# Kernel optimization log

Hardware: AMD Instinct MI355X
Metric: run time of the kernel (lower is better)

The kernel has to match this reference:

```python
import jax, jax.numpy as jnp
import numpy as np

# ---- static problem configuration (matches init_kwargs) ----
N_PAIRS = 256
NODES_PER_GRAPH = 64
EDGES_PER_GRAPH = 200
MAX_EDGES = 256            # max_edge_set_size
N_GRAPHS = 2 * N_PAIRS     # query/corpus interleaved
N_NODES = N_GRAPHS * NODES_PER_GRAPH
N_EDGES = N_GRAPHS * EDGES_PER_GRAPH
NODE_DIM = 16
EDGE_DIM = 16
H = 128                    # node_state_dim
E_ENC = 64                 # encoded edge feature dim
MSG = 256                  # edge_hidden_sizes[-1] = 2*H (GMN GRU convention)
SK = 32                    # sinkhorn_feature_dim
PROP_STEPS = 5
SK_ITERS = 20
TEMP = 0.1


def setup_inputs() -> dict:
    key = jax.random.key(0)
    ks = jax.random.split(key, 16)
    node_features = jax.random.normal(ks[0], (N_NODES, NODE_DIM), jnp.float32)
    edge_features = jax.random.normal(ks[1], (N_EDGES, EDGE_DIM), jnp.float32)
    # edges are grouped per graph (graph g owns edges [g*E, (g+1)*E)) and
    # endpoints stay inside graph g's node range, as get_graph_features assumes
    offs = np.repeat(np.arange(N_GRAPHS) * NODES_PER_GRAPH, EDGES_PER_GRAPH)
    rng = np.random.default_rng(0)
    from_idx = jnp.asarray(offs + rng.integers(0, NODES_PER_GRAPH, N_EDGES), jnp.int32)
    to_idx = jnp.asarray(offs + rng.integers(0, NODES_PER_GRAPH, N_EDGES), jnp.int32)

    def lin(k, i, o):
        return jax.random.normal(k, (i, o), jnp.float32) / np.sqrt(i).astype(np.float32)

    p = dict(
        enc_node_w=lin(ks[2], NODE_DIM, H), enc_node_b=jnp.zeros((H,), jnp.float32),
        enc_edge_w=lin(ks[3], EDGE_DIM, E_ENC), enc_edge_b=jnp.zeros((E_ENC,), jnp.float32),
        msg_w1=lin(ks[4], 2 * H + E_ENC, MSG), msg_b1=jnp.zeros((MSG,), jnp.float32),
        msg_w2=lin(ks[5], MSG, MSG), msg_b2=jnp.zeros((MSG,), jnp.float32),
        rmsg_w1=lin(ks[6], 2 * H + E_ENC, MSG), rmsg_b1=jnp.zeros((MSG,), jnp.float32),
        rmsg_w2=lin(ks[7], MSG, MSG), rmsg_b2=jnp.zeros((MSG,), jnp.float32),
        gru_w_ih=lin(ks[8], MSG, 3 * H), gru_b_ih=jnp.zeros((3 * H,), jnp.float32),
        gru_w_hh=lin(ks[9], H, 3 * H), gru_b_hh=jnp.zeros((3 * H,), jnp.float32),
        sk_w1=lin(ks[10], MSG, SK), sk_b1=jnp.zeros((SK,), jnp.float32),
        sk_w2=lin(ks[11], SK, SK), sk_b2=jnp.zeros((SK,), jnp.float32),
    )
    return {"node_features": node_features, "edge_features": edge_features,
            "from_idx": from_idx, "to_idx": to_idx, **p}


def _mlp2(x, w1, b1, w2, b2):
    # Linear -> ReLU -> Linear (GMN MLP: no activation after last layer)
    return jax.nn.relu(x @ w1 + b1) @ w2 + b2


def reference(node_features, edge_features, from_idx, to_idx,
              enc_node_w, enc_node_b, enc_edge_w, enc_edge_b,
              msg_w1, msg_b1, msg_w2, msg_b2,
              rmsg_w1, rmsg_b1, rmsg_w2, rmsg_b2,
              gru_w_ih, gru_b_ih, gru_w_hh, gru_b_hh,
              sk_w1, sk_b1, sk_w2, sk_b2):
    # ---- GraphEncoder (single-layer MLPs) ----
    h = node_features @ enc_node_w + enc_node_b          # [N_NODES, H]
    e = edge_features @ enc_edge_w + enc_edge_b          # [N_EDGES, E_ENC]

    def edge_msgs(h):
        s, d = h[from_idx], h[to_idx]                    # gathers [N_EDGES, H]
        fwd = _mlp2(jnp.concatenate([s, d, e], axis=1), msg_w1, msg_b1, msg_w2, msg_b2)
        rev = _mlp2(jnp.concatenate([d, s, e], axis=1), rmsg_w1, rmsg_b1, rmsg_w2, rmsg_b2)
        return fwd, rev                                  # [N_EDGES, MSG] each

    # ---- propagation loop: gather -> edge MLP -> scatter -> GRU update ----
    for _ in range(PROP_STEPS):
        fwd, rev = edge_msgs(h)
        agg = (jax.ops.segment_sum(fwd, to_idx, num_segments=N_NODES)
               + jax.ops.segment_sum(rev, from_idx, num_segments=N_NODES))  # [N_NODES, MSG]
        gi = agg @ gru_w_ih + gru_b_ih                   # [N_NODES, 3H]
        gh = h @ gru_w_hh + gru_b_hh
        r = jax.nn.sigmoid(gi[:, :H] + gh[:, :H])
        z = jax.nn.sigmoid(gi[:, H:2 * H] + gh[:, H:2 * H])
        n = jnp.tanh(gi[:, 2 * H:] + r * gh[:, 2 * H:])
        h = (1.0 - z) * n + z * h                        # torch GRU update

    # ---- propagation_messages: per-edge fwd + rev message ----
    fwd, rev = edge_msgs(h)
    e_final = fwd + rev                                  # [N_EDGES, MSG]

    # ---- split_and_stack: per-graph edge sets padded to MAX_EDGES ----
    stacked = jnp.pad(e_final.reshape(N_GRAPHS, EDGES_PER_GRAPH, MSG),
                      ((0, 0), (0, MAX_EDGES - EDGES_PER_GRAPH), (0, 0)))
    q, c = stacked[0::2], stacked[1::2]                  # [B, MAX_EDGES, MSG]

    # ---- sinkhorn feature MLP + size mask ----
    tq = _mlp2(q, sk_w1, sk_b1, sk_w2, sk_b2)            # [B, MAX_EDGES, SK]
    tc = _mlp2(c, sk_w1, sk_b1, sk_w2, sk_b2)
    mask = (jnp.arange(MAX_EDGES) < EDGES_PER_GRAPH).astype(jnp.float32)[None, :, None]
    mq, mc = mask * tq, mask * tc

    # ---- log-domain Sinkhorn ----
    la = jnp.einsum('bif,bjf->bij', mq, mc) / TEMP       # [B, MAX_EDGES, MAX_EDGES]
    for _ in range(SK_ITERS):
        la = la - jax.nn.logsumexp(la, axis=2, keepdims=True)
        la = la - jax.nn.logsumexp(la, axis=1, keepdims=True)
    plan = jnp.exp(la)

    # ---- feature_alignment_score: -sum relu(q - P @ c) ----
    return -jnp.sum(jax.nn.relu(q - jnp.einsum('bij,bjf->bif', plan, c)), axis=(1, 2))
```

## Files before the change

kernel.cpp:

```cpp
#include <hip/hip_runtime.h>
#include <math.h>

typedef __attribute__((ext_vector_type(4))) float f32x4;
typedef __attribute__((ext_vector_type(8))) short s16x8;
typedef __attribute__((ext_vector_type(4))) short s16x4;

#define NN 32768
#define NE 102400
#define HD 128
#define EED 64
#define MSGD 256
#define NG 512
#define EPG 200
#define NP 256
#define SKD 32

__device__ inline short f2bf(float x){
  union{float f; unsigned u;} z; z.f=x;
  unsigned r = (z.u + 0x7fffu + ((z.u>>16)&1u)) >> 16;
  return (short)r;
}
__device__ inline float bf2f(unsigned short u){
  union{unsigned u; float f;} z; z.u = ((unsigned)u)<<16; return z.f;
}
__device__ inline float frcp(float x){
  float r; asm("v_rcp_f32 %0, %1" : "=v"(r) : "v"(x)); return r;
}

__global__ void __launch_bounds__(256) k_enc_node(const float* __restrict__ nf,
    const float* __restrict__ W, const float* __restrict__ b,
    float* __restrict__ h, short* __restrict__ hb){
  __shared__ float Ws[16*128];
  int t = threadIdx.x;
  for (int i=t;i<16*128;i+=256) Ws[i]=W[i];
  __syncthreads();
  int node = blockIdx.x*2 + (t>>7);
  int f = t & 127;
  const float* x = nf + node*16;
  float acc = b[f];
  #pragma unroll
  for (int k=0;k<16;k++) acc = fmaf(x[k], Ws[k*128+f], acc);
  h[node*HD+f] = acc;
  hb[node*HD+f] = f2bf(acc);
}

__global__ void __launch_bounds__(256) k_enc_edge(const float* __restrict__ ef,
    const float* __restrict__ W, const float* __restrict__ b, short* __restrict__ eeb){
  __shared__ float Ws[16*64];
  int t = threadIdx.x;
  for (int i=t;i<16*64;i+=256) Ws[i]=W[i];
  __syncthreads();
  int edge = blockIdx.x*4 + (t>>6);
  int f = t & 63;
  const float* x = ef + edge*16;
  float acc = b[f];
  #pragma unroll
  for (int k=0;k<16;k++) acc = fmaf(x[k], Ws[k*64+f], acc);
  eeb[edge*EED+f] = f2bf(acc);
}

__global__ void __launch_bounds__(256) k_pack(const float* __restrict__ W,
    short* __restrict__ dst, int K, int N){
  int NT = N >> 4;
  int i = blockIdx.x*256 + threadIdx.x;
  if (i >= (K/32)*NT*64) return;
  int l = i & 63, tile = i >> 6;
  int nt = tile % NT, kt = tile / NT;
  int lr = l & 15, lq = l >> 4;
  s16x8 v;
  #pragma unroll
  for (int j=0;j<8;j++)
    v[j] = f2bf(W[(size_t)(kt*32 + lq*8 + j)*N + nt*16 + lr]);
  *((s16x8*)dst + i) = v;
}

__global__ void __launch_bounds__(256) k_csr_count(const int* __restrict__ fidx,
    const int* __restrict__ tidx, int* __restrict__ cur_in, int* __restrict__ cur_out){
  int e = blockIdx.x*256 + threadIdx.x;
  if (e >= NE) return;
  atomicAdd(&cur_in[tidx[e]], 1);
  atomicAdd(&cur_out[fidx[e]], 1);
}
__global__ void k_csr_scan(int* __restrict__ cur_in, int* __restrict__ start_in,
    int* __restrict__ cur_out, int* __restrict__ start_out){
  if (threadIdx.x) return;
  int g = blockIdx.x;
  int n0 = g*64, base = g*EPG;
  int run = base;
  for (int i=0;i<64;i++){ int c=cur_in[n0+i]; start_in[n0+i]=run; cur_in[n0+i]=run; run+=c; }
  run = base;
  for (int i=0;i<64;i++){ int c=cur_out[n0+i]; start_out[n0+i]=run; cur_out[n0+i]=run; run+=c; }
}
__global__ void __launch_bounds__(256) k_csr_fill(const int* __restrict__ fidx,
    const int* __restrict__ tidx, int* __restrict__ cur_in, int* __restrict__ cur_out,
    int* __restrict__ list_in, int* __restrict__ list_out){
  int e = blockIdx.x*256 + threadIdx.x;
  if (e >= NE) return;
  int p1 = atomicAdd(&cur_in[tidx[e]], 1);  list_in[p1] = e;
  int p2 = atomicAdd(&cur_out[fidx[e]], 1); list_out[p2] = e;
}

__global__ void __launch_bounds__(256,2) k_msg_both(const short* __restrict__ hb,
    const short* __restrict__ eeb, const int* __restrict__ from_idx, const int* __restrict__ to_idx,
    const short* __restrict__ w1f, const float* __restrict__ b1f,
    const short* __restrict__ w2f, const float* __restrict__ b2f,
    const short* __restrict__ w1r, const float* __restrict__ b1r,
    const short* __restrict__ w2r, const float* __restrict__ b2r,
    short* __restrict__ mf, short* __restrict__ mr){
  __shared__ __align__(16) short Xs[64][328];
  __shared__ __align__(16) short Ys[64][264];
  __shared__ int sidx[64], didx[64];
  int t = threadIdx.x;
  int e0 = blockIdx.x*64;
  if (t < 64){ sidx[t]=from_idx[e0+t]; didx[t]=to_idx[e0+t]; }
  __syncthreads();
  for (int i=t; i<64*40; i+=256){
    int r = i/40, c8 = (i - r*40)*8;
    const short* src;
    if (c8 < 128)      src = hb + (size_t)sidx[r]*HD + c8;
    else if (c8 < 256) src = hb + (size_t)didx[r]*HD + (c8-128);
    else               src = eeb + (size_t)(e0+r)*EED + (c8-256);
    *(s16x8*)&Xs[r][c8] = *(const s16x8*)src;
  }
  __syncthreads();

  int wv = t>>6, l = t&63, lr = l&15, lq = l>>4;
  int cbase = wv*64;

  for (int dir=0; dir<2; dir++){
    const s16x8* W1v = (const s16x8*)(dir ? w1r : w1f);
    const float* B1  = dir ? b1r : b1f;
    const s16x8* W2v = (const s16x8*)(dir ? w2r : w2f);
    const float* B2  = dir ? b2r : b2f;

    f32x4 acc[4][4];
    #pragma unroll
    for (int ct=0; ct<4; ct++){
      float bb = B1[cbase + ct*16 + lr];
      #pragma unroll
      for (int rt=0; rt<4; rt++) acc[rt][ct] = (f32x4){bb,bb,bb,bb};
    }
    {
      s16x8 a0[4], b0[4], b1[4];
      int sc0 = dir ? 4 : 0;
      #pragma unroll
      for (int rt=0;rt<4;rt++) a0[rt] = *(const s16x8*)&Xs[rt*16+lr][sc0*32 + lq*8];
      #pragma unroll
      for (int ct=0;ct<4;ct++) b0[ct] = W1v[(size_t)(0*16 + wv*4 + ct)*64 + l];
      #pragma unroll
      for (int ct=0;ct<4;ct++) b1[ct] = W1v[(size_t)(1*16 + wv*4 + ct)*64 + l];
      #pragma unroll
      for (int kt=0; kt<10; kt++){
        s16x8 an[4], bn[4];
        if (kt < 9){
          int sc = (dir && (kt+1)<8) ? ((kt+1)^4) : (kt+1);
          #pragma unroll
          for (int rt=0;rt<4;rt++) an[rt] = *(const s16x8*)&Xs[rt*16+lr][sc*32 + lq*8];
        }
        if (kt < 8){
          #pragma unroll
          for (int ct=0;ct<4;ct++) bn[ct] = W1v[(size_t)((kt+2)*16 + wv*4 + ct)*64 + l];
        }
        #pragma unroll
        for (int rt=0; rt<4; rt++)
          #pragma unroll
          for (int ct=0; ct<4; ct++)
            acc[rt][ct] = __builtin_amdgcn_mfma_f32_16x16x32_bf16(a0[rt], b0[ct], acc[rt][ct], 0,0,0);
        #pragma unroll
        for (int i=0;i<4;i++){ a0[i]=an[i]; b0[i]=b1[i]; b1[i]=bn[i]; }
      }
    }
    #pragma unroll
    for (int rt=0; rt<4; rt++)
      #pragma unroll
      for (int ct=0; ct<4; ct++)
        #pragma unroll
        for (int r=0; r<4; r++)
          Ys[rt*16 + lq*4 + r][cbase + ct*16 + lr] = f2bf(fmaxf(acc[rt][ct][r], 0.f));
    __syncthreads();

    f32x4 acc2[4][4];
    #pragma unroll
    for (int ct=0; ct<4; ct++){
      float bb = B2[cbase + ct*16 + lr];
      #pragma unroll
      for (int rt=0; rt<4; rt++) acc2[rt][ct] = (f32x4){bb,bb,bb,bb};
    }
    {
      s16x8 a0[4], b0[4], b1[4];
      #pragma unroll
      for (int rt=0;rt<4;rt++) a0[rt] = *(const s16x8*)&Ys[rt*16+lr][lq*8];
      #pragma unroll
      for (int ct=0;ct<4;ct++) b0[ct] = W2v[(size_t)(0*16 + wv*4 + ct)*64 + l];
      #pragma unroll
      for (int ct=0;ct<4;ct++) b1[ct] = W2v[(size_t)(1*16 + wv*4 + ct)*64 + l];
      #pragma unroll
      for (int kt=0; kt<8; kt++){
        s16x8 an[4], bn[4];
        if (kt < 7){
          #pragma unroll
          for (int rt=0;rt<4;rt++) an[rt] = *(const s16x8*)&Ys[rt*16+lr][(kt+1)*32 + lq*8];
        }
        if (kt < 6){
          #pragma unroll
          for (int ct=0;ct<4;ct++) bn[ct] = W2v[(size_t)((kt+2)*16 + wv*4 + ct)*64 + l];
        }
        #pragma unroll
        for (int rt=0; rt<4; rt++)
          #pragma unroll
          for (int ct=0; ct<4; ct++)
            acc2[rt][ct] = __builtin_amdgcn_mfma_f32_16x16x32_bf16(a0[rt], b0[ct], acc2[rt][ct], 0,0,0);
        #pragma unroll
        for (int i=0;i<4;i++){ a0[i]=an[i]; b0[i]=b1[i]; b1[i]=bn[i]; }
      }
    }
    __syncthreads();
    #pragma unroll
    for (int rt=0; rt<4; rt++)
      #pragma unroll
      for (int ct=0; ct<4; ct++)
        #pragma unroll
        for (int r=0; r<4; r++)
          Ys[rt*16 + lq*4 + r][cbase + ct*16 + lr] = f2bf(acc2[rt][ct][r]);
    __syncthreads();
    {
      short* dst = (dir ? mr : mf) + (size_t)e0*MSGD;
      for (int i=t; i<64*32; i+=256){
        int row = i>>5, c8 = (i&31)*8;
        *(s16x8*)&dst[(size_t)row*MSGD + c8] = *(const s16x8*)&Ys[row][c8];
      }
    }
    __syncthreads();
  }
}

__global__ void __launch_bounds__(256) k_gather(const unsigned short* __restrict__ mf,
    const unsigned short* __restrict__ mr,
    const int* __restrict__ start_in, const int* __restrict__ end_in, const int* __restrict__ list_in,
    const int* __restrict__ start_out, const int* __restrict__ end_out, const int* __restrict__ list_out,
    short* __restrict__ aggb){
  int n = blockIdx.x*4 + (threadIdx.x>>6);
  int l = threadIdx.x & 63;
  float4 acc = {0.f,0.f,0.f,0.f};
  int s0 = start_in[n], e0 = end_in[n];
  for (int i=s0; i<e0; i++){
    int e = list_in[i];
    ushort4 v = *(const ushort4*)&mf[(size_t)e*MSGD + 4*l];
    acc.x += bf2f(v.x); acc.y += bf2f(v.y); acc.z += bf2f(v.z); acc.w += bf2f(v.w);
  }
  int s1 = start_out[n], e1 = end_out[n];
  for (int i=s1; i<e1; i++){
    int e = list_out[i];
    ushort4 v = *(const ushort4*)&mr[(size_t)e*MSGD + 4*l];
    acc.x += bf2f(v.x); acc.y += bf2f(v.y); acc.z += bf2f(v.z); acc.w += bf2f(v.w);
  }
  s16x4 o;
  o[0]=f2bf(acc.x); o[1]=f2bf(acc.y); o[2]=f2bf(acc.z); o[3]=f2bf(acc.w);
  *(s16x4*)&aggb[(size_t)n*MSGD + 4*l] = o;
}

__global__ void __launch_bounds__(256,2) k_msg_fin(const short* __restrict__ hb,
    const short* __restrict__ eeb, const int* __restrict__ from_idx, const int* __restrict__ to_idx,
    const short* __restrict__ w1f, const float* __restrict__ b1f,
    const short* __restrict__ w2f, const float* __restrict__ b2f,
    const short* __restrict__ w1r, const float* __restrict__ b1r,
    const short* __restrict__ w2r, const float* __restrict__ b2r,
    short* __restrict__ efb){
  __shared__ __align__(16) short Xs[64][328];
  __shared__ __align__(16) short Ys[64][264];
  __shared__ int sidx[64], didx[64];
  int t = threadIdx.x;
  int e0 = blockIdx.x*64;
  if (t < 64){ sidx[t]=from_idx[e0+t]; didx[t]=to_idx[e0+t]; }
  __syncthreads();
  for (int i=t; i<64*40; i+=256){
    int r = i/40, c8 = (i - r*40)*8;
    const short* src;
    if (c8 < 128)      src = hb + (size_t)sidx[r]*HD + c8;
    else if (c8 < 256) src = hb + (size_t)didx[r]*HD + (c8-128);
    else               src = eeb + (size_t)(e0+r)*EED + (c8-256);
    *(s16x8*)&Xs[r][c8] = *(const s16x8*)src;
  }
  __syncthreads();

  int wv = t>>6, l = t&63, lr = l&15, lq = l>>4;
  int cbase = wv*64;
  f32x4 fsv[4][4];

  for (int dir=0; dir<2; dir++){
    const s16x8* W1v = (const s16x8*)(dir ? w1r : w1f);
    const float* B1  = dir ? b1r : b1f;
    const s16x8* W2v = (const s16x8*)(dir ? w2r : w2f);
    const float* B2  = dir ? b2r : b2f;

    f32x4 acc[4][4];
    #pragma unroll
    for (int ct=0; ct<4; ct++){
      float bb = B1[cbase + ct*16 + lr];
      #pragma unroll
      for (int rt=0; rt<4; rt++) acc[rt][ct] = (f32x4){bb,bb,bb,bb};
    }
    {
      s16x8 a0[4], b0[4], b1[4];
      int sc0 = dir ? 4 : 0;
      #pragma unroll
      for (int rt=0;rt<4;rt++) a0[rt] = *(const s16x8*)&Xs[rt*16+lr][sc0*32 + lq*8];
      #pragma unroll
      for (int ct=0;ct<4;ct++) b0[ct] = W1v[(size_t)(0*16 + wv*4 + ct)*64 + l];
      #pragma unroll
      for (int ct=0;ct<4;ct++) b1[ct] = W1v[(size_t)(1*16 + wv*4 + ct)*64 + l];
      #pragma unroll
      for (int kt=0; kt<10; kt++){
        s16x8 an[4], bn[4];
        if (kt < 9){
          int sc = (dir && (kt+1)<8) ? ((kt+1)^4) : (kt+1);
          #pragma unroll
          for (int rt=0;rt<4;rt++) an[rt] = *(const s16x8*)&Xs[rt*16+lr][sc*32 + lq*8];
        }
        if (kt < 8){
          #pragma unroll
          for (int ct=0;ct<4;ct++) bn[ct] = W1v[(size_t)((kt+2)*16 + wv*4 + ct)*64 + l];
        }
        #pragma unroll
        for (int rt=0; rt<4; rt++)
          #pragma unroll
          for (int ct=0; ct<4; ct++)
            acc[rt][ct] = __builtin_amdgcn_mfma_f32_16x16x32_bf16(a0[rt], b0[ct], acc[rt][ct], 0,0,0);
        #pragma unroll
        for (int i=0;i<4;i++){ a0[i]=an[i]; b0[i]=b1[i]; b1[i]=bn[i]; }
      }
    }
    #pragma unroll
    for (int rt=0; rt<4; rt++)
      #pragma unroll
      for (int ct=0; ct<4; ct++)
        #pragma unroll
        for (int r=0; r<4; r++)
          Ys[rt*16 + lq*4 + r][cbase + ct*16 + lr] = f2bf(fmaxf(acc[rt][ct][r], 0.f));
    __syncthreads();

    f32x4 acc2[4][4];
    #pragma unroll
    for (int ct=0; ct<4; ct++){
      float bb = B2[cbase + ct*16 + lr];
      #pragma unroll
      for (int rt=0; rt<4; rt++) acc2[rt][ct] = (f32x4){bb,bb,bb,bb};
    }
    {
      s16x8 a0[4], b0[4], b1[4];
      #pragma unroll
      for (int rt=0;rt<4;rt++) a0[rt] = *(const s16x8*)&Ys[rt*16+lr][lq*8];
      #pragma unroll
      for (int ct=0;ct<4;ct++) b0[ct] = W2v[(size_t)(0*16 + wv*4 + ct)*64 + l];
      #pragma unroll
      for (int ct=0;ct<4;ct++) b1[ct] = W2v[(size_t)(1*16 + wv*4 + ct)*64 + l];
      #pragma unroll
      for (int kt=0; kt<8; kt++){
        s16x8 an[4], bn[4];
        if (kt < 7){
          #pragma unroll
          for (int rt=0;rt<4;rt++) an[rt] = *(const s16x8*)&Ys[rt*16+lr][(kt+1)*32 + lq*8];
        }
        if (kt < 6){
          #pragma unroll
          for (int ct=0;ct<4;ct++) bn[ct] = W2v[(size_t)((kt+2)*16 + wv*4 + ct)*64 + l];
        }
        #pragma unroll
        for (int rt=0; rt<4; rt++)
          #pragma unroll
          for (int ct=0; ct<4; ct++)
            acc2[rt][ct] = __builtin_amdgcn_mfma_f32_16x16x32_bf16(a0[rt], b0[ct], acc2[rt][ct], 0,0,0);
        #pragma unroll
        for (int i=0;i<4;i++){ a0[i]=an[i]; b0[i]=b1[i]; b1[i]=bn[i]; }
      }
    }

    if (dir==0){
      #pragma unroll
      for (int rt=0; rt<4; rt++)
        #pragma unroll
        for (int ct=0; ct<4; ct++) fsv[rt][ct] = acc2[rt][ct];
      __syncthreads();
    } else {
      __syncthreads();
      #pragma unroll
      for (int rt=0; rt<4; rt++)
        #pragma unroll
        for (int ct=0; ct<4; ct++)
          #pragma unroll
          for (int r=0; r<4; r++)
            Ys[rt*16 + lq*4 + r][cbase + ct*16 + lr] = f2bf(fsv[rt][ct][r] + acc2[rt][ct][r]);
      __syncthreads();
      short* dst = efb + (size_t)e0*MSGD;
      for (int i=t; i<64*32; i+=256){
        int row = i>>5, c8 = (i&31)*8;
        *(s16x8*)&dst[(size_t)row*MSGD + c8] = *(const s16x8*)&Ys[row][c8];
      }
    }
  }
}

__global__ void __launch_bounds__(256,2) k_gru(const float* __restrict__ h,
    const short* __restrict__ hb, const short* __restrict__ aggb,
    const short* __restrict__ wih_p, const float* __restrict__ bih,
    const short* __restrict__ whh_p, const float* __restrict__ bhh,
    float* __restrict__ hnew, short* __restrict__ hnewb){
  __shared__ __align__(16) short aggs[64][264];
  __shared__ __align__(16) short hs[64][136];
  int t = threadIdx.x;
  int n0 = blockIdx.x*64;
  for (int i=t; i<64*32; i+=256){
    int r = i>>5, c8 = (i&31)*8;
    *(s16x8*)&aggs[r][c8] = *(const s16x8*)&aggb[(size_t)(n0+r)*MSGD + c8];
  }
  for (int i=t; i<64*16; i+=256){
    int r = i>>4, c8 = (i&15)*8;
    *(s16x8*)&hs[r][c8] = *(const s16x8*)&hb[(size_t)(n0+r)*HD + c8];
  }
  __syncthreads();

  int wv = t>>6, l = t&63, lr = l&15, lq = l>>4;
  const s16x8* Wih_v = (const s16x8*)wih_p;
  const s16x8* Whh_v = (const s16x8*)whh_p;

  f32x4 gi[4][6], gh[4][6];
  #pragma unroll
  for (int ct=0; ct<6; ct++){
    int bcol = (ct>>1)*128 + wv*32 + (ct&1)*16 + lr;
    float bi = bih[bcol], bh = bhh[bcol];
    #pragma unroll
    for (int rt=0; rt<4; rt++){
      gi[rt][ct] = (f32x4){bi,bi,bi,bi};
      gh[rt][ct] = (f32x4){bh,bh,bh,bh};
    }
  }
  for (int kt=0; kt<8; kt++){
    s16x8 af[4], bfr[6];
    #pragma unroll
    for (int rt=0; rt<4; rt++) af[rt] = *(const s16x8*)&aggs[rt*16+lr][kt*32 + lq*8];
    #pragma unroll
    for (int ct=0; ct<6; ct++){
      int nt = (ct>>1)*8 + wv*2 + (ct&1);
      bfr[ct] = Wih_v[(size_t)(kt*24 + nt)*64 + l];
    }
    #pragma unroll
    for (int rt=0; rt<4; rt++)
      #pragma unroll
      for (int ct=0; ct<6; ct++)
        gi[rt][ct] = __builtin_amdgcn_mfma_f32_16x16x32_bf16(af[rt], bfr[ct], gi[rt][ct], 0,0,0);
  }
  for (int kt=0; kt<4; kt++){
    s16x8 af[4], bfr[6];
    #pragma unroll
    for (int rt=0; rt<4; rt++) af[rt] = *(const s16x8*)&hs[rt*16+lr][kt*32 + lq*8];
    #pragma unroll
    for (int ct=0; ct<6; ct++){
      int nt = (ct>>1)*8 + wv*2 + (ct&1);
      bfr[ct] = Whh_v[(size_t)(kt*24 + nt)*64 + l];
    }
    #pragma unroll
    for (int rt=0; rt<4; rt++)
      #pragma unroll
      for (int ct=0; ct<6; ct++)
        gh[rt][ct] = __builtin_amdgcn_mfma_f32_16x16x32_bf16(af[rt], bfr[ct], gh[rt][ct], 0,0,0);
  }
  #pragma unroll
  for (int rt=0; rt<4; rt++)
    #pragma unroll
    for (int j=0; j<2; j++)
      #pragma unroll
      for (int r=0; r<4; r++){
        int row = n0 + rt*16 + lq*4 + r;
        int col = wv*32 + j*16 + lr;
        float rr = 1.f/(1.f + __expf(-(gi[rt][j][r]   + gh[rt][j][r])));
        float zz = 1.f/(1.f + __expf(-(gi[rt][2+j][r] + gh[rt][2+j][r])));
        float gn = gi[rt][4+j][r] + rr*gh[rt][4+j][r];
        float nn = 1.f - 2.f/(__expf(2.f*gn) + 1.f);
        float hold = h[(size_t)row*HD + col];
        float hv = (1.f - zz)*nn + zz*hold;
        hnew[(size_t)row*HD + col] = hv;
        hnewb[(size_t)row*HD + col] = f2bf(hv);
      }
}

__global__ void __launch_bounds__(256,2) k_tall(const short* __restrict__ efb,
    const short* __restrict__ W1p, const float* __restrict__ b1,
    const short* __restrict__ W2p, const float* __restrict__ b2,
    float* __restrict__ tall){
  __shared__ __align__(16) short Xs[64][264];
  __shared__ __align__(16) short Ys[64][40];
  int t = threadIdx.x;
  int g = blockIdx.x>>2, r0 = (blockIdx.x&3)*64;
  for (int i=t; i<64*32; i+=256){
    int r = i>>5, c8 = (i&31)*8;
    int row = r0 + r;
    s16x8 v = (row < EPG) ? *(const s16x8*)&efb[((size_t)g*EPG + row)*MSGD + c8]
                          : (s16x8){0,0,0,0,0,0,0,0};
    *(s16x8*)&Xs[r][c8] = v;
  }
  __syncthreads();
  int wv = t>>6, l = t&63, lr = l&15, lq = l>>4;
  const s16x8* W1v = (const s16x8*)W1p;
  const s16x8* W2v = (const s16x8*)W2p;
  f32x4 acc[2];
  #pragma unroll
  for (int ct=0; ct<2; ct++){
    float bb = b1[ct*16 + lr];
    acc[ct] = (f32x4){bb,bb,bb,bb};
  }
  for (int kt=0; kt<8; kt++){
    s16x8 a = *(const s16x8*)&Xs[wv*16+lr][kt*32 + lq*8];
    #pragma unroll
    for (int ct=0; ct<2; ct++){
      s16x8 bfr = W1v[(size_t)(kt*2 + ct)*64 + l];
      acc[ct] = __builtin_amdgcn_mfma_f32_16x16x32_bf16(a, bfr, acc[ct], 0,0,0);
    }
  }
  #pragma unroll
  for (int ct=0; ct<2; ct++)
    #pragma unroll
    for (int r=0; r<4; r++)
      Ys[wv*16 + lq*4 + r][ct*16 + lr] = f2bf(fmaxf(acc[ct][r], 0.f));
  __syncthreads();
  f32x4 acc2[2];
  #pragma unroll
  for (int ct=0; ct<2; ct++){
    float bb = b2[ct*16 + lr];
    acc2[ct] = (f32x4){bb,bb,bb,bb};
  }
  {
    s16x8 a = *(const s16x8*)&Ys[wv*16+lr][lq*8];
    #pragma unroll
    for (int ct=0; ct<2; ct++){
      s16x8 bfr = W2v[(size_t)ct*64 + l];
      acc2[ct] = __builtin_amdgcn_mfma_f32_16x16x32_bf16(a, bfr, acc2[ct], 0,0,0);
    }
  }
  #pragma unroll
  for (int ct=0; ct<2; ct++)
    #pragma unroll
    for (int r=0; r<4; r++){
      int row = r0 + wv*16 + lq*4 + r;
      tall[((size_t)g*256 + row)*SKD + ct*16 + lr] = (row < EPG) ? acc2[ct][r] : 0.f;
    }
}

__global__ void __attribute__((amdgpu_waves_per_eu(4,4))) __launch_bounds__(1024)
k_sinkhorn(const float* __restrict__ tall, short* __restrict__ plan){
  __shared__ float tqs[256*32];
  __shared__ float tcsT[32*257];
  __shared__ float cv[256];
  __shared__ float psm[16][256];
  int p = blockIdx.x, t = threadIdx.x;
  int w = t>>6, l = t&63;
  int rbase = w*16;
  const float* tq = tall + (size_t)(2*p)*8192;
  const float* tc = tall + (size_t)(2*p+1)*8192;
  for (int i=t; i<8192; i+=1024){
    tqs[i] = tq[i];
    tcsT[(i&31)*257 + (i>>5)] = tc[i];
  }
  __syncthreads();
  float4 E[16];
  #pragma unroll
  for (int k=0; k<16; k++){
    float4 a = {0.f,0.f,0.f,0.f};
    for (int kk=0; kk<32; kk+=4){
      float4 c0 = *(const float4*)&tcsT[(kk+0)*257 + 4*l];
      float4 c1 = *(const float4*)&tcsT[(kk+1)*257 + 4*l];
      float4 c2 = *(const float4*)&tcsT[(kk+2)*257 + 4*l];
      float4 c3 = *(const float4*)&tcsT[(kk+3)*257 + 4*l];
      float4 q = *(const float4*)&tqs[(rbase+k)*32 + kk];
      a.x = fmaf(q.x,c0.x, fmaf(q.y,c1.x, fmaf(q.z,c2.x, fmaf(q.w,c3.x, a.x))));
      a.y = fmaf(q.x,c0.y, fmaf(q.y,c1.y, fmaf(q.z,c2.y, fmaf(q.w,c3.y, a.y))));
      a.z = fmaf(q.x,c0.z, fmaf(q.y,c1.z, fmaf(q.z,c2.z, fmaf(q.w,c3.z, a.z))));
      a.w = fmaf(q.x,c0.w, fmaf(q.y,c1.w, fmaf(q.z,c2.w, fmaf(q.w,c3.w, a.w))));
    }
    a.x *= 10.f; a.y *= 10.f; a.z *= 10.f; a.w *= 10.f;
    float m = fmaxf(fmaxf(a.x,a.y), fmaxf(a.z,a.w));
    #pragma unroll
    for (int off=32; off; off>>=1) m = fmaxf(m, __shfl_xor(m, off));
    float s = __expf(a.x-m)+__expf(a.y-m)+__expf(a.z-m)+__expf(a.w-m);
    #pragma unroll
    for (int off=32; off; off>>=1) s += __shfl_xor(s, off);
    float r = m + __logf(s);
    E[k].x = __expf(a.x - r); E[k].y = __expf(a.y - r);
    E[k].z = __expf(a.z - r); E[k].w = __expf(a.w - r);
  }

  for (int it=0; it<20; it++){
    float4 sm = {0.f,0.f,0.f,0.f};
    #pragma unroll
    for (int k=0;k<16;k++){
      sm.x += E[k].x; sm.y += E[k].y; sm.z += E[k].z; sm.w += E[k].w;
    }
    *(float4*)&psm[w][4*l] = sm;
    __syncthreads();
    if (t < 256){
      float s = psm[0][t];
      #pragma unroll
      for (int ww=1; ww<16; ww++) s += psm[ww][t];
      cv[t] = frcp(s);
    }
    __syncthreads();
    float4 ic = *(const float4*)&cv[4*l];
    #pragma unroll
    for (int k=0;k<16;k++){
      E[k].x *= ic.x; E[k].y *= ic.y; E[k].z *= ic.z; E[k].w *= ic.w;
    }
    if (it < 19){
      #pragma unroll
      for (int k=0;k<16;k++){
        float s = E[k].x + E[k].y + E[k].z + E[k].w;
        #pragma unroll
        for (int off=32; off; off>>=1) s += __shfl_xor(s, off);
        float inv = frcp(s);
        E[k].x *= inv; E[k].y *= inv; E[k].z *= inv; E[k].w *= inv;
      }
    }
  }
  short* P = plan + (size_t)p*65536;
  #pragma unroll
  for (int k=0;k<16;k++){
    s16x4 o;
    o[0]=f2bf(E[k].x); o[1]=f2bf(E[k].y); o[2]=f2bf(E[k].z); o[3]=f2bf(E[k].w);
    *(s16x4*)&P[(size_t)(rbase+k)*256 + 4*l] = o;
  }
}

__global__ void __launch_bounds__(256,2) k_loss(const short* __restrict__ plan,
    const short* __restrict__ efb, float* __restrict__ out){
  __shared__ __align__(16) short Ps[128][40];
  __shared__ __align__(16) short Cs[256][40];
  __shared__ float red[4];
  int t = threadIdx.x;
  int b = blockIdx.x, p = b>>1, rh = b&1;
  int i0 = rh*128;
  int wv = t>>6, l = t&63, lr = l&15, lq = l>>4;
  const short* Pb = plan + (size_t)p*65536;
  const unsigned short* C = (const unsigned short*)(efb + (size_t)(2*p+1)*EPG*MSGD);
  const unsigned short* Q = (const unsigned short*)(efb + (size_t)(2*p)*EPG*MSGD);

  f32x4 acc[2][16];
  #pragma unroll
  for (int rt=0;rt<2;rt++)
    #pragma unroll
    for (int ct=0;ct<16;ct++) acc[rt][ct] = (f32x4){0.f,0.f,0.f,0.f};

  for (int kt=0; kt<8; kt++){
    __syncthreads();
    for (int i=t; i<128*4; i+=256){
      int r = i>>2, c8 = (i&3)*8;
      *(s16x8*)&Ps[r][c8] = *(const s16x8*)&Pb[(size_t)(i0+r)*256 + kt*32 + c8];
    }
    for (int i=t; i<32*64; i+=256){
      int k = i>>6, c4 = (i&63)*4;
      int j = kt*32 + k;
      ushort4 v = (j < EPG) ? *(const ushort4*)&C[(size_t)j*256 + c4] : (ushort4){0,0,0,0};
      Cs[c4+0][k]=(short)v.x; Cs[c4+1][k]=(short)v.y; Cs[c4+2][k]=(short)v.z; Cs[c4+3][k]=(short)v.w;
    }
    __syncthreads();
    s16x8 a0 = *(const s16x8*)&Ps[wv*32      + lr][lq*8];
    s16x8 a1 = *(const s16x8*)&Ps[wv*32 + 16 + lr][lq*8];
    #pragma unroll
    for (int ct=0; ct<16; ct++){
      s16x8 bfr = *(const s16x8*)&Cs[ct*16+lr][lq*8];
      acc[0][ct] = __builtin_amdgcn_mfma_f32_16x16x32_bf16(a0, bfr, acc[0][ct], 0,0,0);
      acc[1][ct] = __builtin_amdgcn_mfma_f32_16x16x32_bf16(a1, bfr, acc[1][ct], 0,0,0);
    }
  }
  float s = 0.f;
  #pragma unroll
  for (int rt=0; rt<2; rt++)
    #pragma unroll
    for (int ct=0; ct<16; ct++)
      #pragma unroll
      for (int r=0; r<4; r++){
        int row = i0 + wv*32 + rt*16 + lq*4 + r;
        int col = ct*16 + lr;
        float q = (row < EPG) ? bf2f(Q[(size_t)row*256 + col]) : 0.f;
        s += fmaxf(q - acc[rt][ct][r], 0.f);
      }
  #pragma unroll
  for (int off=32; off; off>>=1) s += __shfl_xor(s, off);
  if (l==0) red[wv] = s;
  __syncthreads();
  if (t==0) atomicAdd(&out[p], -(red[0]+red[1]+red[2]+red[3]));
}

extern "C" void kernel_launch(void* const* d_in, const int* in_sizes, int n_in,
                              void* d_out, int out_size, void* d_ws, size_t ws_size,
                              hipStream_t stream){
  const float* nf   = (const float*)d_in[0];
  const float* ef   = (const float*)d_in[1];
  const int*   fidx = (const int*)d_in[2];
  const int*   tidx = (const int*)d_in[3];
  const float* enw  = (const float*)d_in[4];
  const float* enb  = (const float*)d_in[5];
  const float* eew  = (const float*)d_in[6];
  const float* eeb_w= (const float*)d_in[7];
  const float* mw1  = (const float*)d_in[8];
  const float* mb1  = (const float*)d_in[9];
  const float* mw2  = (const float*)d_in[10];
  const float* mb2  = (const float*)d_in[11];
  const float* rw1  = (const float*)d_in[12];
  const float* rb1  = (const float*)d_in[13];
  const float* rw2  = (const float*)d_in[14];
  const float* rb2  = (const float*)d_in[15];
  const float* wih  = (const float*)d_in[16];
  const float* bih  = (const float*)d_in[17];
  const float* whh  = (const float*)d_in[18];
  const float* bhh  = (const float*)d_in[19];
  const float* skw1 = (const float*)d_in[20];
  const float* skb1 = (const float*)d_in[21];
  const float* skw2 = (const float*)d_in[22];
  const float* skb2 = (const float*)d_in[23];
  float* out = (float*)d_out;

  float* ws = (float*)d_ws;
  float* h_a   = ws;
  float* h_b   = h_a + (size_t)NN*HD;
  short* hb_a  = (short*)(h_b + (size_t)NN*HD);
  short* hb_b  = hb_a + (size_t)NN*HD;
  short* ee_b  = hb_b + (size_t)NN*HD;
  short* mf    = ee_b + (size_t)NE*EED;
  short* mr    = mf + (size_t)NE*MSGD;
  short* e_finb = mf;
  float* t_all = (float*)(mr + (size_t)NE*MSGD);
  float* la    = t_all + (size_t)NG*256*SKD;

  short* w1f_p = (short*)t_all;
  short* w1r_p = w1f_p + 320*256;
  short* w2f_p = w1r_p + 320*256;
  short* w2r_p = w2f_p + 256*256;
  short* wih_p = w2r_p + 256*256;
  short* whh_p = wih_p + 256*384;
  int*   csr   = (int*)(t_all + 221184);
  int* cur_in    = csr;
  int* cur_out   = cur_in  + NN;
  int* start_in  = cur_out + NN;
  int* start_out = start_in + NN;
  int* list_in   = start_out + NN;
  int* list_out  = list_in + NE;

  short* aggb   = (short*)la;
  short* plan_s = (short*)la;
  short* skw1_p = (short*)(la + 9000000);
  short* skw2_p = skw1_p + 256*32;

  k_pack<<<40, 256, 0, stream>>>(mw1, w1f_p, 320, 256);
  k_pack<<<40, 256, 0, stream>>>(rw1, w1r_p, 320, 256);
  k_pack<<<32, 256, 0, stream>>>(mw2, w2f_p, 256, 256);
  k_pack<<<32, 256, 0, stream>>>(rw2, w2r_p, 256, 256);
  k_pack<<<48, 256, 0, stream>>>(wih, wih_p, 256, 384);
  k_pack<<<24, 256, 0, stream>>>(whh, whh_p, 128, 384);
  k_pack<<<4, 256, 0, stream>>>(skw1, skw1_p, 256, 32);
  k_pack<<<1, 256, 0, stream>>>(skw2, skw2_p, 32, 32);

  k_enc_node<<<NN/2, 256, 0, stream>>>(nf, enw, enb, h_a, hb_a);
  k_enc_edge<<<NE/4, 256, 0, stream>>>(ef, eew, eeb_w, ee_b);

  hipMemsetAsync(csr, 0, (size_t)2*NN*sizeof(int), stream);
  k_csr_count<<<NE/256, 256, 0, stream>>>(fidx, tidx, cur_in, cur_out);
  k_csr_scan<<<NG, 64, 0, stream>>>(cur_in, start_in, cur_out, start_out);
  k_csr_fill<<<NE/256, 256, 0, stream>>>(fidx, tidx, cur_in, cur_out, list_in, list_out);

  float* hc = h_a; float* hn = h_b;
  short* hbc = hb_a; short* hbn = hb_b;
  for (int step=0; step<5; step++){
    k_msg_both<<<NE/64, 256, 0, stream>>>(hbc, ee_b, fidx, tidx,
        w1f_p, mb1, w2f_p, mb2, w1r_p, rb1, w2r_p, rb2, mf, mr);
    k_gather<<<NN/4, 256, 0, stream>>>((const unsigned short*)mf, (const unsigned short*)mr,
        start_in, cur_in, list_in, start_out, cur_out, list_out, aggb);
    k_gru<<<NN/64, 256, 0, stream>>>(hc, hbc, aggb, wih_p, bih, whh_p, bhh, hn, hbn);
    float* tmp = hc; hc = hn; hn = tmp;
    short* tmb = hbc; hbc = hbn; hbn = tmb;
  }
  k_msg_fin<<<NE/64, 256, 0, stream>>>(hbc, ee_b, fidx, tidx,
      w1f_p, mb1, w2f_p, mb2, w1r_p, rb1, w2r_p, rb2, e_finb);

  k_tall<<<NG*4, 256, 0, stream>>>(e_finb, skw1_p, skb1, skw2_p, skb2, t_all);
  k_sinkhorn<<<NP, 1024, 0, stream>>>(t_all, plan_s);

  hipMemsetAsync(out, 0, (size_t)NP*sizeof(float), stream);
  k_loss<<<NP*2, 256, 0, stream>>>(plan_s, e_finb, out);
}
```

Baseline: 1.085 ms.

## Use 8 waves per block in message and GRU kernels, merge msg_fin into template

The edge-message MLP and GRU kernels move from 4 to 8 wavefronts per block, each wave now computing half as many output column tiles, with launch bounds raised to 512 threads and 4 blocks. k_msg_fin is folded into a templated k_msg with a FIN flag. The aim is more waves in flight and lower per-wave register pressure to hide global weight loads and LDS latency. The cost is that each wave reloads the same A fragments from LDS for fewer MFMAs, so LDS traffic per output grows.

Measured after the change: 1.094 ms. No clear change (+0.8%).

```diff
diff --git a/kernel.cpp b/kernel.cpp
--- a/kernel.cpp
+++ b/kernel.cpp
@@ -100,7 +100,8 @@
   int p2 = atomicAdd(&cur_out[fidx[e]], 1); list_out[p2] = e;
 }
 
-__global__ void __launch_bounds__(256,2) k_msg_both(const short* __restrict__ hb,
+template<bool FIN>
+__global__ void __launch_bounds__(512,4) k_msg(const short* __restrict__ hb,
     const short* __restrict__ eeb, const int* __restrict__ from_idx, const int* __restrict__ to_idx,
     const short* __restrict__ w1f, const float* __restrict__ b1f,
     const short* __restrict__ w2f, const float* __restrict__ b2f,
@@ -114,7 +115,7 @@
   int e0 = blockIdx.x*64;
   if (t < 64){ sidx[t]=from_idx[e0+t]; didx[t]=to_idx[e0+t]; }
   __syncthreads();
-  for (int i=t; i<64*40; i+=256){
+  for (int i=t; i<64*40; i+=512){
     int r = i/40, c8 = (i - r*40)*8;
     const short* src;
     if (c8 < 128)      src = hb + (size_t)sidx[r]*HD + c8;
@@ -125,7 +126,8 @@
   __syncthreads();
 
   int wv = t>>6, l = t&63, lr = l&15, lq = l>>4;
-  int cbase = wv*64;
+  int cbase = wv*32;
+  f32x4 fsv[4][2];
 
   for (int dir=0; dir<2; dir++){
     const s16x8* W1v = (const s16x8*)(dir ? w1r : w1f);
@@ -133,25 +135,25 @@
     const s16x8* W2v = (const s16x8*)(dir ? w2r : w2f);
     const float* B2  = dir ? b2r : b2f;
 
-    f32x4 acc[4][4];
-    #pragma unroll
-    for (int ct=0; ct<4; ct++){
+    f32x4 acc[4][2];
+    #pragma unroll
+    for (int ct=0; ct<2; ct++){
       float bb = B1[cbase + ct*16 + lr];
       #pragma unroll
       for (int rt=0; rt<4; rt++) acc[rt][ct] = (f32x4){bb,bb,bb,bb};
     }
     {
-      s16x8 a0[4], b0[4], b1[4];
+      s16x8 a0[4], b0[2], b1[2];
       int sc0 = dir ? 4 : 0;
       #pragma unroll
       for (int rt=0;rt<4;rt++) a0[rt] = *(const s16x8*)&Xs[rt*16+lr][sc0*32 + lq*8];
       #pragma unroll
-      for (int ct=0;ct<4;ct++) b0[ct] = W1v[(size_t)(0*16 + wv*4 + ct)*64 + l];
-      #pragma unroll
-      for (int ct=0;ct<4;ct++) b1[ct] = W1v[(size_t)(1*16 + wv*4 + ct)*64 + l];
+      for (int ct=0;ct<2;ct++) b0[ct] = W1v[(size_t)(0*16 + wv*2 + ct)*64 + l];
+      #pragma unroll
+      for (int ct=0;ct<2;ct++) b1[ct] = W1v[(size_t)(1*16 + wv*2 + ct)*64 + l];
       #pragma unroll
       for (int kt=0; kt<10; kt++){
-        s16x8 an[4], bn[4];
+        s16x8 an[4], bn[2];
         if (kt < 9){
           int sc = (dir && (kt+1)<8) ? ((kt+1)^4) : (kt+1);
           #pragma unroll
@@ -159,78 +161,105 @@
         }
         if (kt < 8){
           #pragma unroll
-          for (int ct=0;ct<4;ct++) bn[ct] = W1v[(size_t)((kt+2)*16 + wv*4 + ct)*64 + l];
+          for (int ct=0;ct<2;ct++) bn[ct] = W1v[(size_t)((kt+2)*16 + wv*2 + ct)*64 + l];
         }
         #pragma unroll
         for (int rt=0; rt<4; rt++)
           #pragma unroll
-          for (int ct=0; ct<4; ct++)
+          for (int ct=0; ct<2; ct++)
             acc[rt][ct] = __builtin_amdgcn_mfma_f32_16x16x32_bf16(a0[rt], b0[ct], acc[rt][ct], 0,0,0);
         #pragma unroll
-        for (int i=0;i<4;i++){ a0[i]=an[i]; b0[i]=b1[i]; b1[i]=bn[i]; }
+        for (int i=0;i<4;i++) a0[i]=an[i];
+        #pragma unroll
+        for (int i=0;i<2;i++){ b0[i]=b1[i]; b1[i]=bn[i]; }
       }
     }
     #pragma unroll
     for (int rt=0; rt<4; rt++)
       #pragma unroll
-      for (int ct=0; ct<4; ct++)
+      for (int ct=0; ct<2; ct++)
         #pragma unroll
         for (int r=0; r<4; r++)
           Ys[rt*16 + lq*4 + r][cbase + ct*16 + lr] = f2bf(fmaxf(acc[rt][ct][r], 0.f));
     __syncthreads();
 
-    f32x4 acc2[4][4];
-    #pragma unroll
-    for (int ct=0; ct<4; ct++){
+    f32x4 acc2[4][2];
+    #pragma unroll
+    for (int ct=0; ct<2; ct++){
       float bb = B2[cbase + ct*16 + lr];
       #pragma unroll
       for (int rt=0; rt<4; rt++) acc2[rt][ct] = (f32x4){bb,bb,bb,bb};
     }
     {
-      s16x8 a0[4], b0[4], b1[4];
+      s16x8 a0[4], b0[2], b1[2];
       #pragma unroll
       for (int rt=0;rt<4;rt++) a0[rt] = *(const s16x8*)&Ys[rt*16+lr][lq*8];
       #pragma unroll
-      for (int ct=0;ct<4;ct++) b0[ct] = W2v[(size_t)(0*16 + wv*4 + ct)*64 + l];
-      #pragma unroll
-      for (int ct=0;ct<4;ct++) b1[ct] = W2v[(size_t)(1*16 + wv*4 + ct)*64 + l];
+      for (int ct=0;ct<2;ct++) b0[ct] = W2v[(size_t)(0*16 + wv*2 + ct)*64 + l];
+      #pragma unroll
+      for (int ct=0;ct<2;ct++) b1[ct] = W2v[(size_t)(1*16 + wv*2 + ct)*64 + l];
       #pragma unroll
       for (int kt=0; kt<8; kt++){
-        s16x8 an[4], bn[4];
+        s16x8 an[4], bn[2];
         if (kt < 7){
           #pragma unroll
           for (int rt=0;rt<4;rt++) an[rt] = *(const s16x8*)&Ys[rt*16+lr][(kt+1)*32 + lq*8];
         }
         if (kt < 6){
           #pragma unroll
-          for (int ct=0;ct<4;ct++) bn[ct] = W2v[(size_t)((kt+2)*16 + wv*4 + ct)*64 + l];
+          for (int ct=0;ct<2;ct++) bn[ct] = W2v[(size_t)((kt+2)*16 + wv*2 + ct)*64 + l];
         }
         #pragma unroll
         for (int rt=0; rt<4; rt++)
           #pragma unroll
-          for (int ct=0; ct<4; ct++)
+          for (int ct=0; ct<2; ct++)
             acc2[rt][ct] = __builtin_amdgcn_mfma_f32_16x16x32_bf16(a0[rt], b0[ct], acc2[rt][ct], 0,0,0);
         #pragma unroll
-        for (int i=0;i<4;i++){ a0[i]=an[i]; b0[i]=b1[i]; b1[i]=bn[i]; }
+        for (int i=0;i<4;i++) a0[i]=an[i];
+        #pragma unroll
+        for (int i=0;i<2;i++){ b0[i]=b1[i]; b1[i]=bn[i]; }
       }
     }
-    __syncthreads();
-    #pragma unroll
-    for (int rt=0; rt<4; rt++)
-      #pragma unroll
-      for (int ct=0; ct<4; ct++)
-        #pragma unroll
-        for (int r=0; r<4; r++)
-          Ys[rt*16 + lq*4 + r][cbase + ct*16 + lr] = f2bf(acc2[rt][ct][r]);
-    __syncthreads();
-    {
+    if (!FIN){
+      __syncthreads();
+      #pragma unroll
+      for (int rt=0; rt<4; rt++)
+        #pragma unroll
+        for (int ct=0; ct<2; ct++)
+          #pragma unroll
+          for (int r=0; r<4; r++)
+            Ys[rt*16 + lq*4 + r][cbase + ct*16 + lr] = f2bf(acc2[rt][ct][r]);
+      __syncthreads();
       short* dst = (dir ? mr : mf) + (size_t)e0*MSGD;
-      for (int i=t; i<64*32; i+=256){
+      for (int i=t; i<64*32; i+=512){
         int row = i>>5, c8 = (i&31)*8;
         *(s16x8*)&dst[(size_t)row*MSGD + c8] = *(const s16x8*)&Ys[row][c8];
       }
-    }
-    __syncthreads();
+      __syncthreads();
+    } else {
+      if (dir==0){
+        #pragma unroll
+        for (int rt=0; rt<4; rt++)
+          #pragma unroll
+          for (int ct=0; ct<2; ct++) fsv[rt][ct] = acc2[rt][ct];
+        __syncthreads();
+      } else {
+        __syncthreads();
+        #pragma unroll
+        for (int rt=0; rt<4; rt++)
+          #pragma unroll
+          for (int ct=0; ct<2; ct++)
+            #pragma unroll
+            for (int r=0; r<4; r++)
+              Ys[rt*16 + lq*4 + r][cbase + ct*16 + lr] = f2bf(fsv[rt][ct][r] + acc2[rt][ct][r]);
+        __syncthreads();
+        short* dst = mf + (size_t)e0*MSGD;
+        for (int i=t; i<64*32; i+=512){
+          int row = i>>5, c8 = (i&31)*8;
+          *(s16x8*)&dst[(size_t)row*MSGD + c8] = *(const s16x8*)&Ys[row][c8];
+        }
+      }
+    }
   }
 }
 
@@ -259,148 +288,7 @@
   *(s16x4*)&aggb[(size_t)n*MSGD + 4*l] = o;
 }
 
-__global__ void __launch_bounds__(256,2) k_msg_fin(const short* __restrict__ hb,
-    const short* __restrict__ eeb, const int* __restrict__ from_idx, const int* __restrict__ to_idx,
-    const short* __restrict__ w1f, const float* __restrict__ b1f,
-    const short* __restrict__ w2f, const float* __restrict__ b2f,
-    const short* __restrict__ w1r, const float* __restrict__ b1r,
-    const short* __restrict__ w2r, const float* __restrict__ b2r,
-    short* __restrict__ efb){
-  __shared__ __align__(16) short Xs[64][328];
-  __shared__ __align__(16) short Ys[64][264];
-  __shared__ int sidx[64], didx[64];
-  int t = threadIdx.x;
-  int e0 = blockIdx.x*64;
-  if (t < 64){ sidx[t]=from_idx[e0+t]; didx[t]=to_idx[e0+t]; }
-  __syncthreads();
-  for (int i=t; i<64*40; i+=256){
-    int r = i/40, c8 = (i - r*40)*8;
-    const short* src;
-    if (c8 < 128)      src = hb + (size_t)sidx[r]*HD + c8;
-    else if (c8 < 256) src = hb + (size_t)didx[r]*HD + (c8-128);
-    else               src = eeb + (size_t)(e0+r)*EED + (c8-256);
-    *(s16x8*)&Xs[r][c8] = *(const s16x8*)src;
-  }
-  __syncthreads();
-
-  int wv = t>>6, l = t&63, lr = l&15, lq = l>>4;
-  int cbase = wv*64;
-  f32x4 fsv[4][4];
-
-  for (int dir=0; dir<2; dir++){
-    const s16x8* W1v = (const s16x8*)(dir ? w1r : w1f);
-    const float* B1  = dir ? b1r : b1f;
-    const s16x8* W2v = (const s16x8*)(dir ? w2r : w2f);
-    const float* B2  = dir ? b2r : b2f;
-
-    f32x4 acc[4][4];
-    #pragma unroll
-    for (int ct=0; ct<4; ct++){
-      float bb = B1[cbase + ct*16 + lr];
-      #pragma unroll
-      for (int rt=0; rt<4; rt++) acc[rt][ct] = (f32x4){bb,bb,bb,bb};
-    }
-    {
-      s16x8 a0[4], b0[4], b1[4];
-      int sc0 = dir ? 4 : 0;
-      #pragma unroll
-      for (int rt=0;rt<4;rt++) a0[rt] = *(const s16x8*)&Xs[rt*16+lr][sc0*32 + lq*8];
-      #pragma unroll
-      for (int ct=0;ct<4;ct++) b0[ct] = W1v[(size_t)(0*16 + wv*4 + ct)*64 + l];
-      #pragma unroll
-      for (int ct=0;ct<4;ct++) b1[ct] = W1v[(size_t)(1*16 + wv*4 + ct)*64 + l];
-      #pragma unroll
-      for (int kt=0; kt<10; kt++){
-        s16x8 an[4], bn[4];
-        if (kt < 9){
-          int sc = (dir && (kt+1)<8) ? ((kt+1)^4) : (kt+1);
-          #pragma unroll
-          for (int rt=0;rt<4;rt++) an[rt] = *(const s16x8*)&Xs[rt*16+lr][sc*32 + lq*8];
-        }
-        if (kt < 8){
-          #pragma unroll
-          for (int ct=0;ct<4;ct++) bn[ct] = W1v[(size_t)((kt+2)*16 + wv*4 + ct)*64 + l];
-        }
-        #pragma unroll
-        for (int rt=0; rt<4; rt++)
-          #pragma unroll
-          for (int ct=0; ct<4; ct++)
-            acc[rt][ct] = __builtin_amdgcn_mfma_f32_16x16x32_bf16(a0[rt], b0[ct], acc[rt][ct], 0,0,0);
-        #pragma unroll
-        for (int i=0;i<4;i++){ a0[i]=an[i]; b0[i]=b1[i]; b1[i]=bn[i]; }
-      }
-    }
-    #pragma unroll
-    for (int rt=0; rt<4; rt++)
-      #pragma unroll
-      for (int ct=0; ct<4; ct++)
-        #pragma unroll
-        for (int r=0; r<4; r++)
-          Ys[rt*16 + lq*4 + r][cbase + ct*16 + lr] = f2bf(fmaxf(acc[rt][ct][r], 0.f));
-    __syncthreads();
-
-    f32x4 acc2[4][4];
-    #pragma unroll
-    for (int ct=0; ct<4; ct++){
-      float bb = B2[cbase + ct*16 + lr];
-      #pragma unroll
-      for (int rt=0; rt<4; rt++) acc2[rt][ct] = (f32x4){bb,bb,bb,bb};
-    }
-    {
-      s16x8 a0[4], b0[4], b1[4];
-      #pragma unroll
-      for (int rt=0;rt<4;rt++) a0[rt] = *(const s16x8*)&Ys[rt*16+lr][lq*8];
-      #pragma unroll
-      for (int ct=0;ct<4;ct++) b0[ct] = W2v[(size_t)(0*16 + wv*4 + ct)*64 + l];
-      #pragma unroll
-      for (int ct=0;ct<4;ct++) b1[ct] = W2v[(size_t)(1*16 + wv*4 + ct)*64 + l];
-      #pragma unroll
-      for (int kt=0; kt<8; kt++){
-        s16x8 an[4], bn[4];
-        if (kt < 7){
-          #pragma unroll
-          for (int rt=0;rt<4;rt++) an[rt] = *(const s16x8*)&Ys[rt*16+lr][(kt+1)*32 + lq*8];
-        }
-        if (kt < 6){
-          #pragma unroll
-          for (int ct=0;ct<4;ct++) bn[ct] = W2v[(size_t)((kt+2)*16 + wv*4 + ct)*64 + l];
-        }
-        #pragma unroll
-        for (int rt=0; rt<4; rt++)
-          #pragma unroll
-          for (int ct=0; ct<4; ct++)
-            acc2[rt][ct] = __builtin_amdgcn_mfma_f32_16x16x32_bf16(a0[rt], b0[ct], acc2[rt][ct], 0,0,0);
-        #pragma unroll
-        for (int i=0;i<4;i++){ a0[i]=an[i]; b0[i]=b1[i]; b1[i]=bn[i]; }
-      }
-    }
-
-    if (dir==0){
-      #pragma unroll
-      for (int rt=0; rt<4; rt++)
-        #pragma unroll
-        for (int ct=0; ct<4; ct++) fsv[rt][ct] = acc2[rt][ct];
-      __syncthreads();
-    } else {
-      __syncthreads();
-      #pragma unroll
-      for (int rt=0; rt<4; rt++)
-        #pragma unroll
-        for (int ct=0; ct<4; ct++)
-          #pragma unroll
-          for (int r=0; r<4; r++)
-            Ys[rt*16 + lq*4 + r][cbase + ct*16 + lr] = f2bf(fsv[rt][ct][r] + acc2[rt][ct][r]);
-      __syncthreads();
-      short* dst = efb + (size_t)e0*MSGD;
-      for (int i=t; i<64*32; i+=256){
-        int row = i>>5, c8 = (i&31)*8;
-        *(s16x8*)&dst[(size_t)row*MSGD + c8] = *(const s16x8*)&Ys[row][c8];
-      }
-    }
-  }
-}
-
-__global__ void __launch_bounds__(256,2) k_gru(const float* __restrict__ h,
+__global__ void __launch_bounds__(512,4) k_gru(const float* __restrict__ h,
     const short* __restrict__ hb, const short* __restrict__ aggb,
     const short* __restrict__ wih_p, const float* __restrict__ bih,
     const short* __restrict__ whh_p, const float* __restrict__ bhh,
@@ -409,11 +297,11 @@
   __shared__ __align__(16) short hs[64][136];
   int t = threadIdx.x;
   int n0 = blockIdx.x*64;
-  for (int i=t; i<64*32; i+=256){
+  for (int i=t; i<64*32; i+=512){
     int r = i>>5, c8 = (i&31)*8;
     *(s16x8*)&aggs[r][c8] = *(const s16x8*)&aggb[(size_t)(n0+r)*MSGD + c8];
   }
-  for (int i=t; i<64*16; i+=256){
+  for (int i=t; i<64*16; i+=512){
     int r = i>>4, c8 = (i&15)*8;
     *(s16x8*)&hs[r][c8] = *(const s16x8*)&hb[(size_t)(n0+r)*HD + c8];
   }
@@ -423,10 +311,10 @@
   const s16x8* Wih_v = (const s16x8*)wih_p;
   const s16x8* Whh_v = (const s16x8*)whh_p;
 
-  f32x4 gi[4][6], gh[4][6];
-  #pragma unroll
-  for (int ct=0; ct<6; ct++){
-    int bcol = (ct>>1)*128 + wv*32 + (ct&1)*16 + lr;
+  f32x4 gi[4][3], gh[4][3];
+  #pragma unroll
+  for (int ct=0; ct<3; ct++){
+    int bcol = ct*128 + wv*16 + lr;
     float bi = bih[bcol], bh = bhh[bcol];
     #pragma unroll
     for (int rt=0; rt<4; rt++){
@@ -435,52 +323,46 @@
     }
   }
   for (int kt=0; kt<8; kt++){
-    s16x8 af[4], bfr[6];
+    s16x8 af[4], bfr[3];
     #pragma unroll
     for (int rt=0; rt<4; rt++) af[rt] = *(const s16x8*)&aggs[rt*16+lr][kt*32 + lq*8];
     #pragma unroll
-    for (int ct=0; ct<6; ct++){
-      int nt = (ct>>1)*8 + wv*2 + (ct&1);
-      bfr[ct] = Wih_v[(size_t)(kt*24 + nt)*64 + l];
-    }
+    for (int ct=0; ct<3; ct++)
+      bfr[ct] = Wih_v[(size_t)(kt*24 + ct*8 + wv)*64 + l];
     #pragma unroll
     for (int rt=0; rt<4; rt++)
       #pragma unroll
-      for (int ct=0; ct<6; ct++)
+      for (int ct=0; ct<3; ct++)
         gi[rt][ct] = __builtin_amdgcn_mfma_f32_16x16x32_bf16(af[rt], bfr[ct], gi[rt][ct], 0,0,0);
   }
   for (int kt=0; kt<4; kt++){
-    s16x8 af[4], bfr[6];
+    s16x8 af[4], bfr[3];
     #pragma unroll
     for (int rt=0; rt<4; rt++) af[rt] = *(const s16x8*)&hs[rt*16+lr][kt*32 + lq*8];
     #pragma unroll
-    for (int ct=0; ct<6; ct++){
-      int nt = (ct>>1)*8 + wv*2 + (ct&1);
-      bfr[ct] = Whh_v[(size_t)(kt*24 + nt)*64 + l];
-    }
+    for (int ct=0; ct<3; ct++)
+      bfr[ct] = Whh_v[(size_t)(kt*24 + ct*8 + wv)*64 + l];
     #pragma unroll
     for (int rt=0; rt<4; rt++)
       #pragma unroll
-      for (int ct=0; ct<6; ct++)
+      for (int ct=0; ct<3; ct++)
         gh[rt][ct] = __builtin_amdgcn_mfma_f32_16x16x32_bf16(af[rt], bfr[ct], gh[rt][ct], 0,0,0);
   }
   #pragma unroll
   for (int rt=0; rt<4; rt++)
     #pragma unroll
-    for (int j=0; j<2; j++)
-      #pragma unroll
-      for (int r=0; r<4; r++){
-        int row = n0 + rt*16 + lq*4 + r;
-        int col = wv*32 + j*16 + lr;
-        float rr = 1.f/(1.f + __expf(-(gi[rt][j][r]   + gh[rt][j][r])));
-        float zz = 1.f/(1.f + __expf(-(gi[rt][2+j][r] + gh[rt][2+j][r])));
-        float gn = gi[rt][4+j][r] + rr*gh[rt][4+j][r];
-        float nn = 1.f - 2.f/(__expf(2.f*gn) + 1.f);
-        float hold = h[(size_t)row*HD + col];
-        float hv = (1.f - zz)*nn + zz*hold;
-        hnew[(size_t)row*HD + col] = hv;
-        hnewb[(size_t)row*HD + col] = f2bf(hv);
-      }
+    for (int r=0; r<4; r++){
+      int row = n0 + rt*16 + lq*4 + r;
+      int col = wv*16 + lr;
+      float rr = 1.f/(1.f + __expf(-(gi[rt][0][r] + gh[rt][0][r])));
+      float zz = 1.f/(1.f + __expf(-(gi[rt][1][r] + gh[rt][1][r])));
+      float gn = gi[rt][2][r] + rr*gh[rt][2][r];
+      float nn = 1.f - 2.f/(__expf(2.f*gn) + 1.f);
+      float hold = h[(size_t)row*HD + col];
+      float hv = (1.f - zz)*nn + zz*hold;
+      hnew[(size_t)row*HD + col] = hv;
+      hnewb[(size_t)row*HD + col] = f2bf(hv);
+    }
 }
 
 __global__ void __launch_bounds__(256,2) k_tall(const short* __restrict__ efb,
@@ -768,16 +650,16 @@
   float* hc = h_a; float* hn = h_b;
   short* hbc = hb_a; short* hbn = hb_b;
   for (int step=0; step<5; step++){
-    k_msg_both<<<NE/64, 256, 0, stream>>>(hbc, ee_b, fidx, tidx,
+    k_msg<false><<<NE/64, 512, 0, stream>>>(hbc, ee_b, fidx, tidx,
         w1f_p, mb1, w2f_p, mb2, w1r_p, rb1, w2r_p, rb2, mf, mr);
     k_gather<<<NN/4, 256, 0, stream>>>((const unsigned short*)mf, (const unsigned short*)mr,
         start_in, cur_in, list_in, start_out, cur_out, list_out, aggb);
-    k_gru<<<NN/64, 256, 0, stream>>>(hc, hbc, aggb, wih_p, bih, whh_p, bhh, hn, hbn);
+    k_gru<<<NN/64, 512, 0, stream>>>(hc, hbc, aggb, wih_p, bih, whh_p, bhh, hn, hbn);
     float* tmp = hc; hc = hn; hn = tmp;
     short* tmb = hbc; hbc = hbn; hbn = tmb;
   }
-  k_msg_fin<<<NE/64, 256, 0, stream>>>(hbc, ee_b, fidx, tidx,
-      w1f_p, mb1, w2f_p, mb2, w1r_p, rb1, w2r_p, rb2, e_finb);
+  k_msg<true><<<NE/64, 512, 0, stream>>>(hbc, ee_b, fidx, tidx,
+      w1f_p, mb1, w2f_p, mb2, w1r_p, rb1, w2r_p, rb2, e_finb, mr);
 
   k_tall<<<NG*4, 256, 0, stream>>>(e_finb, skw1_p, skb1, skw2_p, skb2, t_all);
   k_sinkhorn<<<NP, 1024, 0, stream>>>(t_all, plan_s);
```
